# Kernel optimization log

Measured on AMD Instinct MI355X. Metric: run time of the kernel, lower is better.

## Reference

```python
import jax, jax.numpy as jnp
import numpy as np

NUM_LAYERS = 25
INPUT = 500
HIDDEN = 64
SEQ = 25
BATCH = 4096
OUT = 10
GATES = 4 * HIDDEN


def setup_inputs() -> dict:
    key = jax.random.key(0)
    ks = jax.random.split(key, 11)
    s = 0.1  # ~ uniform(-1/sqrt(H),1/sqrt(H)) scale used by torch LSTM init
    return {
        "x": jax.random.normal(ks[0], (SEQ, BATCH, INPUT), jnp.float32),
        "W_ih0": jax.random.normal(ks[1], (GATES, INPUT), jnp.float32) * s,
        "W_hh0": jax.random.normal(ks[2], (GATES, HIDDEN), jnp.float32) * s,
        "b_ih0": jax.random.normal(ks[3], (GATES,), jnp.float32) * s,
        "b_hh0": jax.random.normal(ks[4], (GATES,), jnp.float32) * s,
        "W_ih_rest": jax.random.normal(ks[5], (NUM_LAYERS - 1, GATES, HIDDEN), jnp.float32) * s,
        "W_hh_rest": jax.random.normal(ks[6], (NUM_LAYERS - 1, GATES, HIDDEN), jnp.float32) * s,
        "b_ih_rest": jax.random.normal(ks[7], (NUM_LAYERS - 1, GATES), jnp.float32) * s,
        "b_hh_rest": jax.random.normal(ks[8], (NUM_LAYERS - 1, GATES), jnp.float32) * s,
        "W_lin": jax.random.normal(ks[9], (OUT, HIDDEN), jnp.float32) * s,
        "b_lin": jax.random.normal(ks[10], (OUT,), jnp.float32) * s,
    }


def _lstm_layer(seq, Wih, Whh, bih, bhh):
    # seq: [T, B, D_in] -> (outputs [T, B, H], h_T [B, H], c_T [B, H])
    T, B, _ = seq.shape
    H = Whh.shape[1]
    # precompute input projection for all timesteps in one big GEMM
    xp = jnp.einsum('tbi,gi->tbg', seq, Wih) + bih + bhh  # [T, B, 4H]
    h0 = jnp.zeros((B, H), seq.dtype)
    c0 = jnp.zeros((B, H), seq.dtype)

    def step(carry, xpt):
        h, c = carry
        g = xpt + h @ Whh.T  # [B, 4H], torch gate order i, f, g, o
        i, f, gg, o = jnp.split(g, 4, axis=-1)
        c = jax.nn.sigmoid(f) * c + jax.nn.sigmoid(i) * jnp.tanh(gg)
        h = jax.nn.sigmoid(o) * jnp.tanh(c)
        return (h, c), h

    (hT, cT), hs = jax.lax.scan(step, (h0, c0), xp)
    return hs, hT, cT


def reference(x, W_ih0, W_hh0, b_ih0, b_hh0, W_ih_rest, W_hh_rest, b_ih_rest, b_hh_rest, W_lin, b_lin):
    hs, hT, cT = _lstm_layer(x, W_ih0, W_hh0, b_ih0, b_hh0)
    h_list, c_list = [hT], [cT]
    for l in range(NUM_LAYERS - 1):  # fixed small layer count: Python loop ok
        hs, hT, cT = _lstm_layer(hs, W_ih_rest[l], W_hh_rest[l], b_ih_rest[l], b_hh_rest[l])
        h_list.append(hT)
        c_list.append(cT)
    h_n = jnp.stack(h_list)  # [L, B, H]
    c_n = jnp.stack(c_list)  # [L, B, H]
    # faithful to torch: out[:, -1, :] indexes the BATCH dim -> [T, H]
    lstm_out = hs[:, -1, :] @ W_lin.T + b_lin  # [T, OUT]
    return (lstm_out, h_n, c_n)
```

## Files before the change

### kernel.cpp

```cpp
#include <hip/hip_runtime.h>

#define T_SEQ 25
#define NBATCH 4096
#define D_IN 500
#define HID 64
#define NG 256
#define NLAYERS 25
#define NOUT 10

typedef __attribute__((ext_vector_type(8))) short bf16x8;
typedef __attribute__((ext_vector_type(4))) short bf16x4;
typedef __attribute__((ext_vector_type(4))) float f32x4;

#define LOG2E 1.4426950408889634f

#define SLOT 1152
#define RSTRIDE (5*SLOT)
#define WRAP_OFF (3*RSTRIDE)
#define LDS_SHORTS (WRAP_OFF + 25*SLOT)

__device__ __forceinline__ short f2bf(float f) {
    union { float f; unsigned u; } v; v.f = f;
    unsigned u = v.u + 0x7FFFu + ((v.u >> 16) & 1u);
    return (short)(u >> 16);
}
__device__ __forceinline__ float bf2f(short s) {
    union { unsigned u; float f; } v;
    v.u = ((unsigned)(unsigned short)s) << 16;
    return v.f;
}
__device__ __forceinline__ bf16x8 cvt8(f32x4 a, f32x4 b) {
    bf16x8 r;
    r[0]=f2bf(a[0]); r[1]=f2bf(a[1]); r[2]=f2bf(a[2]); r[3]=f2bf(a[3]);
    r[4]=f2bf(b[0]); r[5]=f2bf(b[1]); r[6]=f2bf(b[2]); r[7]=f2bf(b[3]);
    return r;
}

__global__ __launch_bounds__(256)
void prep(const float* __restrict__ Wih0, const float* __restrict__ Whh0,
          const float* __restrict__ WihR, const float* __restrict__ WhhR,
          const float* __restrict__ bihR, const float* __restrict__ bhhR,
          short* __restrict__ wbf2, short* __restrict__ whh0b,
          short* __restrict__ wihRb, short* __restrict__ whhRb,
          float* __restrict__ bsum) {
    int idx = blockIdx.x * 256 + threadIdx.x;
    if (idx < 131072) {
        int j = idx & 7, lane = (idx >> 3) & 63, nt = (idx >> 9) & 15, kc = idx >> 13;
        int n = nt*16 + (lane & 15);
        int k = kc*32 + (lane >> 4)*8 + j;
        wbf2[idx] = (k < D_IN) ? f2bf(Wih0[n * D_IN + k]) : (short)0;
    } else if (idx < 147456) {
        int j = idx - 131072; whh0b[j] = f2bf(Whh0[j]);
    } else if (idx < 540672) {
        int j = idx - 147456; wihRb[j] = f2bf(WihR[j]);
    } else if (idx < 933888) {
        int j = idx - 540672; whhRb[j] = f2bf(WhhR[j]);
    } else if (idx < 940032) {
        int j = idx - 933888; bsum[j] = bihR[j] + bhhR[j];
    }
}

__global__ __launch_bounds__(256, 1)
void xp0_gemm(const float* __restrict__ x, const short* __restrict__ wbf2,
              const float* __restrict__ bih0, const float* __restrict__ bhh0,
              short* __restrict__ xp0b) {
    const int tid = threadIdx.x;
    const int wv = tid >> 6, lane = tid & 63, col = lane & 15, q = lane >> 4;
    const int t  = blockIdx.x >> 5;
    const int b0 = (blockIdx.x & 31) << 7;

    f32x4 acc[2][16];
    #pragma unroll
    for (int nt = 0; nt < 16; nt++) {
        int g = nt*16 + col;
        float bv = bih0[g] + bhh0[g];
        acc[0][nt] = (f32x4){bv,bv,bv,bv};
        acc[1][nt] = acc[0][nt];
    }
    const float* xrow0 = x + ((size_t)t*NBATCH + b0 + wv*32 + col)*D_IN;
    const float* xrow1 = xrow0 + 16*(size_t)D_IN;

    #pragma unroll 3
    for (int kc = 0; kc < 15; kc++) {
        const int ko = kc*32 + q*8;
        const f32x4* p0 = (const f32x4*)(xrow0 + ko);
        const f32x4* p1 = (const f32x4*)(xrow1 + ko);
        bf16x8 a0 = cvt8(p0[0], p0[1]);
        bf16x8 a1 = cvt8(p1[0], p1[1]);
        #pragma unroll
        for (int nt = 0; nt < 16; nt++) {
            bf16x8 bfr = *(const bf16x8*)(wbf2 + ((size_t)(kc*16+nt)*64 + lane)*8);
            acc[0][nt] = __builtin_amdgcn_mfma_f32_16x16x32_bf16(a0, bfr, acc[0][nt], 0,0,0);
            acc[1][nt] = __builtin_amdgcn_mfma_f32_16x16x32_bf16(a1, bfr, acc[1][nt], 0,0,0);
        }
    }
    {
        f32x4 z = (f32x4){0.f,0.f,0.f,0.f};
        f32x4 lo0=z, hi0=z, lo1=z, hi1=z;
        const int ko = 480 + q*8;
        if (q < 2) {
            lo0 = *(const f32x4*)(xrow0 + ko); hi0 = *(const f32x4*)(xrow0 + ko + 4);
            lo1 = *(const f32x4*)(xrow1 + ko); hi1 = *(const f32x4*)(xrow1 + ko + 4);
        } else if (q == 2) {
            lo0 = *(const f32x4*)(xrow0 + 496);
            lo1 = *(const f32x4*)(xrow1 + 496);
        }
        bf16x8 a0 = cvt8(lo0, hi0);
        bf16x8 a1 = cvt8(lo1, hi1);
        #pragma unroll
        for (int nt = 0; nt < 16; nt++) {
            bf16x8 bfr = *(const bf16x8*)(wbf2 + ((size_t)(15*16+nt)*64 + lane)*8);
            acc[0][nt] = __builtin_amdgcn_mfma_f32_16x16x32_bf16(a0, bfr, acc[0][nt], 0,0,0);
            acc[1][nt] = __builtin_amdgcn_mfma_f32_16x16x32_bf16(a1, bfr, acc[1][nt], 0,0,0);
        }
    }
    #pragma unroll
    for (int ms = 0; ms < 2; ms++) {
        #pragma unroll
        for (int nt = 0; nt < 16; nt++) {
            int g = nt*16 + col;
            int b = b0 + wv*32 + ms*16 + q*4;
            bf16x4 o;
            o[0]=f2bf(acc[ms][nt][0]); o[1]=f2bf(acc[ms][nt][1]);
            o[2]=f2bf(acc[ms][nt][2]); o[3]=f2bf(acc[ms][nt][3]);
            *(bf16x4*)(xp0b + ((size_t)t*NG + g)*NBATCH + b) = o;
        }
    }
}

__global__ __launch_bounds__(1024, 4)
void lstm_persist(const short* __restrict__ whh0b, const short* __restrict__ wihRb,
                  const short* __restrict__ whhRb, const float* __restrict__ bsum,
                  const float* __restrict__ Wlin, const float* __restrict__ blin,
                  const short* __restrict__ xp0b, float* __restrict__ out) {
    __shared__ short lds[LDS_SHORTS];
    __shared__ float h24[T_SEQ*HID];
    const int tid = threadIdx.x;
    const int w = tid >> 6, lane = tid & 63, col = lane & 15, q = lane >> 4;
    const int g = w >> 2;
    const int hh = (w & 3)*16 + col;
    const int b0 = blockIdx.x << 4;
    float* __restrict__ h_n = out + 250;
    float* __restrict__ c_n = h_n + (size_t)NLAYERS*NBATCH*HID;

    bf16x8 wih[4][2], whh[4][2];
    float bias[4];
    float c4[4] = {0.f,0.f,0.f,0.f};
    bf16x4 xpn[4];

    if (g == 0) {
        #pragma unroll
        for (int gt = 0; gt < 4; gt++) {
            const short* wr = whh0b + (size_t)(gt*64 + hh)*64;
            whh[gt][0] = *(const bf16x8*)(wr + q*8);
            whh[gt][1] = *(const bf16x8*)(wr + 32 + q*8);
            wih[gt][0] = whh[gt][0]; wih[gt][1] = whh[gt][1];
            bias[gt] = 0.f;
            xpn[gt] = *(const bf16x4*)(xp0b + (size_t)(gt*64 + hh)*NBATCH + b0 + q*4);
        }
    } else {
        const short* wi = wihRb + (size_t)(g-1)*16384;
        const short* wh = whhRb + (size_t)(g-1)*16384;
        #pragma unroll
        for (int gt = 0; gt < 4; gt++) {
            int gg = gt*64 + hh;
            wih[gt][0] = *(const bf16x8*)(wi + (size_t)gg*64 + q*8);
            wih[gt][1] = *(const bf16x8*)(wi + (size_t)gg*64 + 32 + q*8);
            whh[gt][0] = *(const bf16x8*)(wh + (size_t)gg*64 + q*8);
            whh[gt][1] = *(const bf16x8*)(wh + (size_t)gg*64 + 32 + q*8);
            bias[gt] = bsum[(size_t)(g-1)*NG + gg];
        }
    }

    int pass = 0, tt = -g, s5 = 0;
    #pragma unroll 1
    for (int s = 0; s < 175; s++) {
        const int l = 4*pass + g;
        if (tt >= 0 && l <= 24) {
            const int t = tt;
            f32x4 acc[4];
            if (l == 0) {
                #pragma unroll
                for (int gt = 0; gt < 4; gt++) {
                    f32x4 p;
                    p[0]=bf2f(xpn[gt][0]); p[1]=bf2f(xpn[gt][1]);
                    p[2]=bf2f(xpn[gt][2]); p[3]=bf2f(xpn[gt][3]);
                    acc[gt] = p;
                }
                if (t < 24) {
                    #pragma unroll
                    for (int gt = 0; gt < 4; gt++)
                        xpn[gt] = *(const bf16x4*)(xp0b +
                            ((size_t)(t+1)*NG + gt*64 + hh)*NBATCH + b0 + q*4);
                }
            } else {
                #pragma unroll
                for (int gt = 0; gt < 4; gt++)
                    acc[gt] = (f32x4){bias[gt],bias[gt],bias[gt],bias[gt]};
                const int inb = (g == 0 ? WRAP_OFF + t*SLOT
                                        : (g-1)*RSTRIDE + s5*SLOT) + col*72;
                bf16x8 a0 = *(const bf16x8*)&lds[inb + q*8];
                bf16x8 a1 = *(const bf16x8*)&lds[inb + 32 + q*8];
                #pragma unroll
                for (int gt = 0; gt < 4; gt++) {
                    acc[gt] = __builtin_amdgcn_mfma_f32_16x16x32_bf16(a0, wih[gt][0], acc[gt], 0,0,0);
                    acc[gt] = __builtin_amdgcn_mfma_f32_16x16x32_bf16(a1, wih[gt][1], acc[gt], 0,0,0);
                }
            }
            if (t > 0) {
                const int p5 = (s5 == 0) ? 4 : s5 - 1;
                const int rb = (g == 3 ? WRAP_OFF + (t-1)*SLOT
                                       : g*RSTRIDE + p5*SLOT) + col*72;
                bf16x8 h0 = *(const bf16x8*)&lds[rb + q*8];
                bf16x8 h1 = *(const bf16x8*)&lds[rb + 32 + q*8];
                #pragma unroll
                for (int gt = 0; gt < 4; gt++) {
                    acc[gt] = __builtin_amdgcn_mfma_f32_16x16x32_bf16(h0, whh[gt][0], acc[gt], 0,0,0);
                    acc[gt] = __builtin_amdgcn_mfma_f32_16x16x32_bf16(h1, whh[gt][1], acc[gt], 0,0,0);
                }
            }
            const int ob = (g == 3 ? WRAP_OFF + t*SLOT : g*RSTRIDE + s5*SLOT);
            #pragma unroll
            for (int rr = 0; rr < 4; rr++) {
                float iv = acc[0][rr], fv = acc[1][rr];
                float gv = acc[2][rr], ov = acc[3][rr];
                float gc = fminf(fmaxf(gv, -30.f), 30.f);
                float ei = __builtin_amdgcn_exp2f(-LOG2E * iv);
                float eg = __builtin_amdgcn_exp2f((2.f*LOG2E) * gc);
                float ef = __builtin_amdgcn_exp2f(-LOG2E * fv);
                float it = (eg - 1.f) *
                    __builtin_amdgcn_rcpf((1.f + ei) * (1.f + eg));
                float cn = __builtin_amdgcn_rcpf(1.f + ef) * c4[rr] + it;
                c4[rr] = cn;
                float cc = fminf(fmaxf(cn, -30.f), 30.f);
                float eo = __builtin_amdgcn_exp2f(-LOG2E * ov);
                float ec = __builtin_amdgcn_exp2f((2.f*LOG2E) * cc);
                float hn = (ec - 1.f) *
                    __builtin_amdgcn_rcpf((1.f + eo) * (1.f + ec));
                lds[ob + (q*4+rr)*72 + hh] = f2bf(hn);
                if (t == 24) {
                    size_t oi = ((size_t)l*NBATCH + b0 + q*4 + rr)*HID + hh;
                    h_n[oi] = hn; c_n[oi] = cn;
                }
                if (l == 24 && q == 3 && rr == 3)
                    h24[t*HID + hh] = hn;
            }
            if (t == 24) {
                const int nl = l + 4;
                if (nl <= 24) {
                    const short* wi = wihRb + (size_t)(nl-1)*16384;
                    const short* wh = whhRb + (size_t)(nl-1)*16384;
                    #pragma unroll
                    for (int gt = 0; gt < 4; gt++) {
                        int gg = gt*64 + hh;
                        wih[gt][0] = *(const bf16x8*)(wi + (size_t)gg*64 + q*8);
                        wih[gt][1] = *(const bf16x8*)(wi + (size_t)gg*64 + 32 + q*8);
                        whh[gt][0] = *(const bf16x8*)(wh + (size_t)gg*64 + q*8);
                        whh[gt][1] = *(const bf16x8*)(wh + (size_t)gg*64 + 32 + q*8);
                        bias[gt] = bsum[(size_t)(nl-1)*NG + gg];
                    }
                }
                c4[0]=c4[1]=c4[2]=c4[3]=0.f;
            }
        }
        __syncthreads();
        tt++;
        if (tt == 25) { tt = 0; pass++; s5 = 0; }
        else if (tt > 0) { s5++; if (s5 == 5) s5 = 0; }
    }

    if (blockIdx.x == 255 && tid < T_SEQ*NOUT) {
        int ti = tid / NOUT, o = tid - ti*NOUT;
        float sacc = blin[o];
        #pragma unroll
        for (int k = 0; k < HID; k++)
            sacc += h24[ti*HID + k] * Wlin[o*HID + k];
        out[tid] = sacc;
    }
}

extern "C" void kernel_launch(void* const* d_in, const int* in_sizes, int n_in,
                              void* d_out, int out_size, void* d_ws, size_t ws_size,
                              hipStream_t stream) {
    const float* x    = (const float*)d_in[0];
    const float* Wih0 = (const float*)d_in[1];
    const float* Whh0 = (const float*)d_in[2];
    const float* bih0 = (const float*)d_in[3];
    const float* bhh0 = (const float*)d_in[4];
    const float* WihR = (const float*)d_in[5];
    const float* WhhR = (const float*)d_in[6];
    const float* bihR = (const float*)d_in[7];
    const float* bhhR = (const float*)d_in[8];
    const float* Wlin = (const float*)d_in[9];
    const float* blin = (const float*)d_in[10];
    float* out = (float*)d_out;

    short* xp0b  = (short*)d_ws;
    short* wbf2  = xp0b  + 26214400;
    short* whh0b = wbf2  + 131072;
    short* wihRb = whh0b + 16384;
    short* whhRb = wihRb + 393216;
    float* bsum  = (float*)(whhRb + 393216);

    prep<<<dim3(3672), dim3(256), 0, stream>>>(Wih0, Whh0, WihR, WhhR, bihR, bhhR,
                                               wbf2, whh0b, wihRb, whhRb, bsum);
    xp0_gemm<<<dim3(800), dim3(256), 0, stream>>>(x, wbf2, bih0, bhh0, xp0b);
    lstm_persist<<<dim3(NBATCH/16), dim3(1024), 0, stream>>>(
        whh0b, wihRb, whhRb, bsum, Wlin, blin, xp0b, out);
}
```

Baseline: 889.2 us.

## Halve wavefronts per block, giving each wave two hidden-column chunks

The persistent LSTM kernel drops from 16 to 8 waves per block. Each wave now computes two 16-wide hidden-column chunks, with doubled weight, bias, cell-state and accumulator registers. This cuts the number of waves taking part in each block-wide barrier and lets one A-fragment LDS load feed twice as many MFMAs. The cost is higher register pressure and less thread-level parallelism per block, which could lower occupancy or cause spills.

```diff
diff --git a/kernel.cpp b/kernel.cpp
--- a/kernel.cpp
+++ b/kernel.cpp
@@ -128,7 +128,7 @@
     }
 }
 
-__global__ __launch_bounds__(1024, 4)
+__global__ __launch_bounds__(512, 2)
 void lstm_persist(const short* __restrict__ whh0b, const short* __restrict__ wihRb,
                   const short* __restrict__ whhRb, const float* __restrict__ bsum,
                   const float* __restrict__ Wlin, const float* __restrict__ blin,
@@ -137,38 +137,49 @@
     __shared__ float h24[T_SEQ*HID];
     const int tid = threadIdx.x;
     const int w = tid >> 6, lane = tid & 63, col = lane & 15, q = lane >> 4;
-    const int g = w >> 2;
-    const int hh = (w & 3)*16 + col;
+    const int g = w >> 1;
+    const int v = w & 1;
     const int b0 = blockIdx.x << 4;
     float* __restrict__ h_n = out + 250;
     float* __restrict__ c_n = h_n + (size_t)NLAYERS*NBATCH*HID;
 
-    bf16x8 wih[4][2], whh[4][2];
-    float bias[4];
-    float c4[4] = {0.f,0.f,0.f,0.f};
-    bf16x4 xpn[4];
+    bf16x8 wih[4][2][2], whh[4][2][2];
+    float bias[4][2];
+    float c8[2][4];
+    bf16x4 xpn[4][2];
+
+    #pragma unroll
+    for (int hc = 0; hc < 2; hc++)
+        #pragma unroll
+        for (int rr = 0; rr < 4; rr++) c8[hc][rr] = 0.f;
 
     if (g == 0) {
         #pragma unroll
-        for (int gt = 0; gt < 4; gt++) {
-            const short* wr = whh0b + (size_t)(gt*64 + hh)*64;
-            whh[gt][0] = *(const bf16x8*)(wr + q*8);
-            whh[gt][1] = *(const bf16x8*)(wr + 32 + q*8);
-            wih[gt][0] = whh[gt][0]; wih[gt][1] = whh[gt][1];
-            bias[gt] = 0.f;
-            xpn[gt] = *(const bf16x4*)(xp0b + (size_t)(gt*64 + hh)*NBATCH + b0 + q*4);
+        for (int gt = 0; gt < 4; gt++)
+        #pragma unroll
+        for (int hc = 0; hc < 2; hc++) {
+            int row = gt*64 + v*32 + hc*16 + col;
+            const short* wr = whh0b + (size_t)row*64;
+            whh[gt][hc][0] = *(const bf16x8*)(wr + q*8);
+            whh[gt][hc][1] = *(const bf16x8*)(wr + 32 + q*8);
+            wih[gt][hc][0] = whh[gt][hc][0];
+            wih[gt][hc][1] = whh[gt][hc][1];
+            bias[gt][hc] = 0.f;
+            xpn[gt][hc] = *(const bf16x4*)(xp0b + (size_t)row*NBATCH + b0 + q*4);
         }
     } else {
         const short* wi = wihRb + (size_t)(g-1)*16384;
         const short* wh = whhRb + (size_t)(g-1)*16384;
         #pragma unroll
-        for (int gt = 0; gt < 4; gt++) {
-            int gg = gt*64 + hh;
-            wih[gt][0] = *(const bf16x8*)(wi + (size_t)gg*64 + q*8);
-            wih[gt][1] = *(const bf16x8*)(wi + (size_t)gg*64 + 32 + q*8);
-            whh[gt][0] = *(const bf16x8*)(wh + (size_t)gg*64 + q*8);
-            whh[gt][1] = *(const bf16x8*)(wh + (size_t)gg*64 + 32 + q*8);
-            bias[gt] = bsum[(size_t)(g-1)*NG + gg];
+        for (int gt = 0; gt < 4; gt++)
+        #pragma unroll
+        for (int hc = 0; hc < 2; hc++) {
+            int row = gt*64 + v*32 + hc*16 + col;
+            wih[gt][hc][0] = *(const bf16x8*)(wi + (size_t)row*64 + q*8);
+            wih[gt][hc][1] = *(const bf16x8*)(wi + (size_t)row*64 + 32 + q*8);
+            whh[gt][hc][0] = *(const bf16x8*)(wh + (size_t)row*64 + q*8);
+            whh[gt][hc][1] = *(const bf16x8*)(wh + (size_t)row*64 + 32 + q*8);
+            bias[gt][hc] = bsum[(size_t)(g-1)*NG + row];
         }
     }
 
@@ -178,33 +189,38 @@
         const int l = 4*pass + g;
         if (tt >= 0 && l <= 24) {
             const int t = tt;
-            f32x4 acc[4];
+            f32x4 acc[4][2];
             if (l == 0) {
                 #pragma unroll
-                for (int gt = 0; gt < 4; gt++) {
+                for (int gt = 0; gt < 4; gt++)
+                #pragma unroll
+                for (int hc = 0; hc < 2; hc++) {
                     f32x4 p;
-                    p[0]=bf2f(xpn[gt][0]); p[1]=bf2f(xpn[gt][1]);
-                    p[2]=bf2f(xpn[gt][2]); p[3]=bf2f(xpn[gt][3]);
-                    acc[gt] = p;
+                    p[0]=bf2f(xpn[gt][hc][0]); p[1]=bf2f(xpn[gt][hc][1]);
+                    p[2]=bf2f(xpn[gt][hc][2]); p[3]=bf2f(xpn[gt][hc][3]);
+                    acc[gt][hc] = p;
                 }
                 if (t < 24) {
                     #pragma unroll
                     for (int gt = 0; gt < 4; gt++)
-                        xpn[gt] = *(const bf16x4*)(xp0b +
-                            ((size_t)(t+1)*NG + gt*64 + hh)*NBATCH + b0 + q*4);
+                    #pragma unroll
+                    for (int hc = 0; hc < 2; hc++)
+                        xpn[gt][hc] = *(const bf16x4*)(xp0b +
+                            ((size_t)(t+1)*NG + gt*64 + v*32 + hc*16 + col)*NBATCH + b0 + q*4);
                 }
             } else {
-                #pragma unroll
-                for (int gt = 0; gt < 4; gt++)
-                    acc[gt] = (f32x4){bias[gt],bias[gt],bias[gt],bias[gt]};
                 const int inb = (g == 0 ? WRAP_OFF + t*SLOT
                                         : (g-1)*RSTRIDE + s5*SLOT) + col*72;
                 bf16x8 a0 = *(const bf16x8*)&lds[inb + q*8];
                 bf16x8 a1 = *(const bf16x8*)&lds[inb + 32 + q*8];
                 #pragma unroll
-                for (int gt = 0; gt < 4; gt++) {
-                    acc[gt] = __builtin_amdgcn_mfma_f32_16x16x32_bf16(a0, wih[gt][0], acc[gt], 0,0,0);
-                    acc[gt] = __builtin_amdgcn_mfma_f32_16x16x32_bf16(a1, wih[gt][1], acc[gt], 0,0,0);
+                for (int gt = 0; gt < 4; gt++)
+                #pragma unroll
+                for (int hc = 0; hc < 2; hc++) {
+                    f32x4 a = (f32x4){bias[gt][hc],bias[gt][hc],bias[gt][hc],bias[gt][hc]};
+                    a = __builtin_amdgcn_mfma_f32_16x16x32_bf16(a0, wih[gt][hc][0], a, 0,0,0);
+                    a = __builtin_amdgcn_mfma_f32_16x16x32_bf16(a1, wih[gt][hc][1], a, 0,0,0);
+                    acc[gt][hc] = a;
                 }
             }
             if (t > 0) {
@@ -214,36 +230,42 @@
                 bf16x8 h0 = *(const bf16x8*)&lds[rb + q*8];
                 bf16x8 h1 = *(const bf16x8*)&lds[rb + 32 + q*8];
                 #pragma unroll
-                for (int gt = 0; gt < 4; gt++) {
-                    acc[gt] = __builtin_amdgcn_mfma_f32_16x16x32_bf16(h0, whh[gt][0], acc[gt], 0,0,0);
-                    acc[gt] = __builtin_amdgcn_mfma_f32_16x16x32_bf16(h1, whh[gt][1], acc[gt], 0,0,0);
+                for (int gt = 0; gt < 4; gt++)
+                #pragma unroll
+                for (int hc = 0; hc < 2; hc++) {
+                    acc[gt][hc] = __builtin_amdgcn_mfma_f32_16x16x32_bf16(h0, whh[gt][hc][0], acc[gt][hc], 0,0,0);
+                    acc[gt][hc] = __builtin_amdgcn_mfma_f32_16x16x32_bf16(h1, whh[gt][hc][1], acc[gt][hc], 0,0,0);
                 }
             }
             const int ob = (g == 3 ? WRAP_OFF + t*SLOT : g*RSTRIDE + s5*SLOT);
             #pragma unroll
-            for (int rr = 0; rr < 4; rr++) {
-                float iv = acc[0][rr], fv = acc[1][rr];
-                float gv = acc[2][rr], ov = acc[3][rr];
-                float gc = fminf(fmaxf(gv, -30.f), 30.f);
-                float ei = __builtin_amdgcn_exp2f(-LOG2E * iv);
-                float eg = __builtin_amdgcn_exp2f((2.f*LOG2E) * gc);
-                float ef = __builtin_amdgcn_exp2f(-LOG2E * fv);
-                float it = (eg - 1.f) *
-                    __builtin_amdgcn_rcpf((1.f + ei) * (1.f + eg));
-                float cn = __builtin_amdgcn_rcpf(1.f + ef) * c4[rr] + it;
-                c4[rr] = cn;
-                float cc = fminf(fmaxf(cn, -30.f), 30.f);
-                float eo = __builtin_amdgcn_exp2f(-LOG2E * ov);
-                float ec = __builtin_amdgcn_exp2f((2.f*LOG2E) * cc);
-                float hn = (ec - 1.f) *
-                    __builtin_amdgcn_rcpf((1.f + eo) * (1.f + ec));
-                lds[ob + (q*4+rr)*72 + hh] = f2bf(hn);
-                if (t == 24) {
-                    size_t oi = ((size_t)l*NBATCH + b0 + q*4 + rr)*HID + hh;
-                    h_n[oi] = hn; c_n[oi] = cn;
-                }
-                if (l == 24 && q == 3 && rr == 3)
-                    h24[t*HID + hh] = hn;
+            for (int hc = 0; hc < 2; hc++) {
+                const int hh = v*32 + hc*16 + col;
+                #pragma unroll
+                for (int rr = 0; rr < 4; rr++) {
+                    float iv = acc[0][hc][rr], fv = acc[1][hc][rr];
+                    float gv = acc[2][hc][rr], ov = acc[3][hc][rr];
+                    float gc = fminf(fmaxf(gv, -30.f), 30.f);
+                    float ei = __builtin_amdgcn_exp2f(-LOG2E * iv);
+                    float eg = __builtin_amdgcn_exp2f((2.f*LOG2E) * gc);
+                    float ef = __builtin_amdgcn_exp2f(-LOG2E * fv);
+                    float it = (eg - 1.f) *
+                        __builtin_amdgcn_rcpf((1.f + ei) * (1.f + eg));
+                    float cn = __builtin_amdgcn_rcpf(1.f + ef) * c8[hc][rr] + it;
+                    c8[hc][rr] = cn;
+                    float cc = fminf(fmaxf(cn, -30.f), 30.f);
+                    float eo = __builtin_amdgcn_exp2f(-LOG2E * ov);
+                    float ec = __builtin_amdgcn_exp2f((2.f*LOG2E) * cc);
+                    float hn = (ec - 1.f) *
+                        __builtin_amdgcn_rcpf((1.f + eo) * (1.f + ec));
+                    lds[ob + (q*4+rr)*72 + hh] = f2bf(hn);
+                    if (t == 24) {
+                        size_t oi = ((size_t)l*NBATCH + b0 + q*4 + rr)*HID + hh;
+                        h_n[oi] = hn; c_n[oi] = cn;
+                    }
+                    if (l == 24 && q == 3 && rr == 3)
+                        h24[t*HID + hh] = hn;
+                }
             }
             if (t == 24) {
                 const int nl = l + 4;
@@ -251,16 +273,21 @@
                     const short* wi = wihRb + (size_t)(nl-1)*16384;
                     const short* wh = whhRb + (size_t)(nl-1)*16384;
                     #pragma unroll
-                    for (int gt = 0; gt < 4; gt++) {
-                        int gg = gt*64 + hh;
-                        wih[gt][0] = *(const bf16x8*)(wi + (size_t)gg*64 + q*8);
-                        wih[gt][1] = *(const bf16x8*)(wi + (size_t)gg*64 + 32 + q*8);
-                        whh[gt][0] = *(const bf16x8*)(wh + (size_t)gg*64 + q*8);
-                        whh[gt][1] = *(const bf16x8*)(wh + (size_t)gg*64 + 32 + q*8);
-                        bias[gt] = bsum[(size_t)(nl-1)*NG + gg];
+                    for (int gt = 0; gt < 4; gt++)
+                    #pragma unroll
+                    for (int hc = 0; hc < 2; hc++) {
+                        int row = gt*64 + v*32 + hc*16 + col;
+                        wih[gt][hc][0] = *(const bf16x8*)(wi + (size_t)row*64 + q*8);
+                        wih[gt][hc][1] = *(const bf16x8*)(wi + (size_t)row*64 + 32 + q*8);
+                        whh[gt][hc][0] = *(const bf16x8*)(wh + (size_t)row*64 + q*8);
+                        whh[gt][hc][1] = *(const bf16x8*)(wh + (size_t)row*64 + 32 + q*8);
+                        bias[gt][hc] = bsum[(size_t)(nl-1)*NG + row];
                     }
                 }
-                c4[0]=c4[1]=c4[2]=c4[3]=0.f;
+                #pragma unroll
+                for (int hc = 0; hc < 2; hc++)
+                #pragma unroll
+                for (int rr = 0; rr < 4; rr++) c8[hc][rr] = 0.f;
             }
         }
         __syncthreads();
@@ -305,6 +332,6 @@
     prep<<<dim3(3672), dim3(256), 0, stream>>>(Wih0, Whh0, WihR, WhhR, bihR, bhhR,
                                                wbf2, whh0b, wihRb, whhRb, bsum);
     xp0_gemm<<<dim3(800), dim3(256), 0, stream>>>(x, wbf2, bih0, bhh0, xp0b);
-    lstm_persist<<<dim3(NBATCH/16), dim3(1024), 0, stream>>>(
+    lstm_persist<<<dim3(NBATCH/16), dim3(512), 0, stream>>>(
         whh0b, wihRb, whhRb, bsum, Wlin, blin, xp0b, out);
 }
```

Result: slower. 920.1 us (+3.5%).
